# Kernel optimization log

Hardware: AMD Instinct MI355X
Metric: run time of the kernel (lower is better)

## Reference

```python
import jax, jax.numpy as jnp
import numpy as np

B, T = 8, 4096
EMBED_DIM = 128
ENGRAM_EMBED_DIM = 64
VOCAB_SIZES = [4096, 4096]
MAX_NGRAM = 3
NUM_HEADS = 2
N_STREAMS = 4
KERNEL = 4
TOTAL_NGRAMS = len(VOCAB_SIZES) * NUM_HEADS          # 4
INPUT_DIM = TOTAL_NGRAMS * ENGRAM_EMBED_DIM          # 256
TOTAL_SLOTS = sum(VOCAB_SIZES) * NUM_HEADS           # 16384


def setup_inputs() -> dict:
    key = jax.random.key(0)
    ks = jax.random.split(key, 10)
    x = jax.random.normal(ks[0], (B, T, N_STREAMS, EMBED_DIM), dtype=jnp.float32)
    input_ids = jax.random.randint(ks[1], (B, T), 0, 50257, dtype=jnp.int32)
    multipliers = jax.random.randint(ks[2], (MAX_NGRAM - 1, NUM_HEADS, MAX_NGRAM), 1, 10000, dtype=jnp.int32)
    embedding = jax.random.normal(ks[3], (TOTAL_SLOTS, ENGRAM_EMBED_DIM), dtype=jnp.float32) * 0.02
    val_W = jax.random.normal(ks[4], (EMBED_DIM, INPUT_DIM), dtype=jnp.float32) * 0.05
    val_b = jnp.zeros((EMBED_DIM,), jnp.float32)
    key_W = jax.random.normal(ks[5], (N_STREAMS, EMBED_DIM, INPUT_DIM), dtype=jnp.float32) * 0.05
    key_b = jnp.zeros((N_STREAMS, EMBED_DIM), jnp.float32)
    normq_w = jnp.ones((N_STREAMS, EMBED_DIM), jnp.float32)
    normk_w = jnp.ones((N_STREAMS, EMBED_DIM), jnp.float32)
    conv_w = jax.random.normal(ks[6], (N_STREAMS * EMBED_DIM, 1, KERNEL), dtype=jnp.float32) * 0.1
    convnorm_w = jnp.ones((N_STREAMS, EMBED_DIM), jnp.float32)
    return {"x": x, "input_ids": input_ids, "multipliers": multipliers,
            "embedding": embedding, "val_W": val_W, "val_b": val_b,
            "key_W": key_W, "key_b": key_b, "normq_w": normq_w,
            "normk_w": normk_w, "conv_w": conv_w, "convnorm_w": convnorm_w}


def rmsnorm(v, w):
    # torch nn.RMSNorm default eps = finfo(dtype).eps
    eps = jnp.finfo(v.dtype).eps
    return v * jax.lax.rsqrt(jnp.mean(v * v, axis=-1, keepdims=True) + eps) * w


def hash_ids_fn(input_ids, multipliers):
    padded = jnp.pad(input_ids, ((0, 0), (MAX_NGRAM - 1, 0)))            # [B, T+2]
    windows = jnp.stack([padded[:, i:i + T] for i in range(MAX_NGRAM)], axis=-1)  # [B,T,3]
    hashes = []
    for n_idx in range(MAX_NGRAM - 1):
        ngram_len = n_idx + 2
        grams = windows[:, :, MAX_NGRAM - ngram_len:]                    # [B,T,L]
        mults = multipliers[n_idx, :, :ngram_len]                        # [H,L]
        mixed = grams[:, :, None, :] * mults[None, None, :, :]           # [B,T,H,L]
        h = mixed[..., 0]
        for k in range(1, ngram_len):
            h = jnp.bitwise_xor(h, mixed[..., k])
        hashes.append(h % VOCAB_SIZES[n_idx])                            # [B,T,H]
    return jnp.concatenate(hashes, axis=2)                               # [B,T,4]


def engram_forward(x, input_ids, multipliers, embedding, val_W, val_b,
                   key_W, key_b, normq_w, normk_w, conv_w, convnorm_w):
    hids = hash_ids_fn(input_ids, multipliers)
    offsets = jnp.cumsum(jnp.array([0] + [v for v in VOCAB_SIZES for _ in range(NUM_HEADS)], jnp.int32))[:-1]
    ids = hids + offsets                                                 # [B,T,4]
    emb = embedding[ids].reshape(B, T, INPUT_DIM)                        # [B,T,256]
    v_base = emb @ val_W.T + val_b                                       # [B,T,128]
    k = rmsnorm(jnp.einsum('bte,gde->btgd', emb, key_W) + key_b, normk_w)  # [B,T,G,D]
    q = rmsnorm(x, normq_w)                                              # [B,T,G,D]
    score = jnp.sum(q * k, axis=-1, keepdims=True) / (EMBED_DIM ** 0.5)
    gates = jax.nn.sigmoid(score)                                        # [B,T,G,1]
    v_gated = v_base[:, :, None, :] * gates                              # [B,T,G,D]
    # ShortConv: per-chunk RMSNorm -> causal depthwise conv -> SiLU
    xn = rmsnorm(v_gated, convnorm_w).reshape(B, T, N_STREAMS * EMBED_DIM)
    x_bct = jnp.transpose(xn, (0, 2, 1))                                 # [B,C,T]
    x_bct = jnp.pad(x_bct, ((0, 0), (0, 0), (KERNEL - 1, 0)))            # causal left pad
    y_bct = jax.lax.conv_general_dilated(
        x_bct, conv_w, window_strides=(1,), padding='VALID',
        dimension_numbers=('NCH', 'OIH', 'NCH'),
        feature_group_count=N_STREAMS * EMBED_DIM)                       # [B,C,T]
    y = jax.nn.silu(y_bct)
    y = jnp.transpose(y, (0, 2, 1)).reshape(B, T, N_STREAMS, EMBED_DIM)
    return v_gated + y


def reference(x, input_ids, multipliers, embedding, val_W, val_b,
              key_W, key_b, normq_w, normk_w, conv_w, convnorm_w):
    return engram_forward(x, input_ids, multipliers, embedding, val_W, val_b,
                          key_W, key_b, normq_w, normk_w, conv_w, convnorm_w)
```

## Files before the change

kernel.cpp:

```cpp
#include <hip/hip_runtime.h>
#include <math.h>

#define EPS 1.1920928955078125e-07f

typedef __attribute__((ext_vector_type(8)))  short short8;
typedef __attribute__((ext_vector_type(4)))  short short4v;
typedef __attribute__((ext_vector_type(16))) float floatx16;

__device__ __forceinline__ float4 ld4(const float* __restrict__ p) { return *(const float4* __restrict__)p; }
__device__ __forceinline__ void   st4(float* __restrict__ p, float4 v) { *(float4* __restrict__)p = v; }

__device__ __forceinline__ unsigned short f2bf(float f) {
    union { float f; unsigned u; } v; v.f = f;
    unsigned r = v.u + 0x7fffu + ((v.u >> 16) & 1u);
    return (unsigned short)(r >> 16);
}

__global__ __launch_bounds__(256) void build_wb(const float* __restrict__ val_W,
                                                const float* __restrict__ key_W,
                                                unsigned short* __restrict__ WbF)
{
    int idx  = blockIdx.x * 256 + threadIdx.x;
    int lane = idx & 63;
    int ks   = (idx >> 6) & 15;
    int nt   = idx >> 10;
    int n = (nt << 5) + (lane & 31);
    int k = (ks << 4) + ((lane >> 5) << 3);
    const float* src = (n < 512) ? key_W + (size_t)n * 256 + k
                                 : val_W + (size_t)(n - 512) * 256 + k;
    float4 v0 = ld4(src), v1 = ld4(src + 4);
    unsigned short o[8] = { f2bf(v0.x), f2bf(v0.y), f2bf(v0.z), f2bf(v0.w),
                            f2bf(v1.x), f2bf(v1.y), f2bf(v1.z), f2bf(v1.w) };
    unsigned short* dst = WbF + (size_t)idx * 8;
    *(short4v*)dst       = *(short4v*)&o[0];
    *(short4v*)(dst + 4) = *(short4v*)&o[4];
}

__global__ __launch_bounds__(256) void build_ebf(const float* __restrict__ emb,
                                                 unsigned short* __restrict__ ebf)
{
    int idx = blockIdx.x * 256 + threadIdx.x;
    const float* src = emb + ((size_t)idx << 3);
    float4 v0 = ld4(src), v1 = ld4(src + 4);
    unsigned short o[8] = { f2bf(v0.x), f2bf(v0.y), f2bf(v0.z), f2bf(v0.w),
                            f2bf(v1.x), f2bf(v1.y), f2bf(v1.z), f2bf(v1.w) };
    unsigned short* dst = ebf + ((size_t)idx << 3);
    *(short4v*)dst       = *(short4v*)&o[0];
    *(short4v*)(dst + 4) = *(short4v*)&o[4];
}

__global__ __launch_bounds__(256, 4) void engram_gemm(
    const float* __restrict__ x,
    const int*   __restrict__ input_ids,
    const int*   __restrict__ mult,
    const unsigned short* __restrict__ ebf,
    const float* __restrict__ val_b,
    const float* __restrict__ key_b,
    const float* __restrict__ normq_w,
    const float* __restrict__ normk_w,
    const unsigned short* __restrict__ WbF,
    float* __restrict__ v_base,
    float* __restrict__ Gbuf,
    float* __restrict__ S2buf)
{
    __shared__ int   sids[32][4];
    __shared__ short AD[32 * 260];

    const int tid  = threadIdx.x;
    const int tok0 = blockIdx.x << 5;

    if (tid < 32) {
        int token = tok0 + tid;
        int b = token >> 12, t = token & 4095;
        const int* row = input_ids + (b << 12);
        unsigned g2 = (unsigned)row[t];
        unsigned g1 = (t >= 1) ? (unsigned)row[t - 1] : 0u;
        unsigned g0 = (t >= 2) ? (unsigned)row[t - 2] : 0u;
        sids[tid][0] = (int)(((g1 * (unsigned)mult[0]) ^ (g2 * (unsigned)mult[1])) & 4095u);
        sids[tid][1] = (int)((((g1 * (unsigned)mult[3]) ^ (g2 * (unsigned)mult[4])) & 4095u) + 4096u);
        sids[tid][2] = (int)((((g0 * (unsigned)mult[6]) ^ (g1 * (unsigned)mult[7]) ^ (g2 * (unsigned)mult[8])) & 4095u) + 8192u);
        sids[tid][3] = (int)((((g0 * (unsigned)mult[9]) ^ (g1 * (unsigned)mult[10]) ^ (g2 * (unsigned)mult[11])) & 4095u) + 12288u);
    }
    __syncthreads();

    #pragma unroll
    for (int it = 0; it < 4; ++it) {
        int f = (it << 8) + tid;
        int token = f >> 5, ch = f & 31;
        const unsigned short* src = ebf + ((size_t)sids[token][ch >> 3] << 6) + ((ch & 7) << 3);
        short4v lo = *(const short4v*)src;
        short4v hi = *(const short4v*)(src + 4);
        short* dst = AD + token * 260 + (ch << 3);
        *(short4v*)dst       = lo;
        *(short4v*)(dst + 4) = hi;
    }
    __syncthreads();

    const int lane = tid & 63;
    const int wv   = tid >> 6;
    const int half = lane >> 5;
    const int mrow = lane & 31;

    const short*  Ap = AD + mrow * 260 + (half << 3);
    const float4* Bf = (const float4*)WbF + lane;

    floatx16 acc[5];
    #pragma unroll
    for (int j = 0; j < 5; ++j)
        #pragma unroll
        for (int r = 0; r < 16; ++r) acc[j][r] = 0.f;

    #pragma unroll 2
    for (int ks = 0; ks < 16; ++ks) {
        short4v al = *(const short4v*)(Ap + (ks << 4));
        short4v ah = *(const short4v*)(Ap + (ks << 4) + 4);
        short8 a = { al[0], al[1], al[2], al[3], ah[0], ah[1], ah[2], ah[3] };
        #pragma unroll
        for (int j = 0; j < 5; ++j) {
            union { float4 f; short8 s; } ub;
            ub.f = Bf[(size_t)((((wv + (j << 2)) << 4) + ks) << 6)];
            acc[j] = __builtin_amdgcn_mfma_f32_32x32x16_bf16(a, ub.s, acc[j], 0, 0, 0);
        }
    }

    const int ty = tid >> 4, tx = tid & 15;
    const int tx8 = tx << 3;
    float* D = (float*)AD;
    const int colw = (wv << 5) + mrow;
    const int rb   = half << 2;

    #pragma unroll
    for (int c = 0; c < 5; ++c) {
        float4 xa0, xb0, xa1, xb1;
        if (c < 4) {
            const float* xp0 = x + ((((size_t)(tok0 + (ty << 1))     << 2) + c) << 7) + tx8;
            const float* xp1 = x + ((((size_t)(tok0 + (ty << 1) + 1) << 2) + c) << 7) + tx8;
            xa0 = ld4(xp0); xb0 = ld4(xp0 + 4);
            xa1 = ld4(xp1); xb1 = ld4(xp1 + 4);
        }
        __syncthreads();
        #pragma unroll
        for (int r = 0; r < 16; ++r) {
            int row = (r & 3) + ((r >> 2) << 3) + rb;
            D[row * 130 + colw] = acc[c][r];
        }
        __syncthreads();

        if (c < 4) {
            const int s = c;
            const float* kbp = key_b   + (s << 7) + tx8;
            const float* nqp = normq_w + (s << 7) + tx8;
            const float* nkp = normk_w + (s << 7) + tx8;
            float4 kba = ld4(kbp), kbb = ld4(kbp + 4);
            float4 nqa = ld4(nqp), nqb = ld4(nqp + 4);
            float4 nka = ld4(nkp), nkb = ld4(nkp + 4);
            float kb[8] = {kba.x, kba.y, kba.z, kba.w, kbb.x, kbb.y, kbb.z, kbb.w};
            float nq[8] = {nqa.x, nqa.y, nqa.z, nqa.w, nqb.x, nqb.y, nqb.z, nqb.w};
            float nk[8] = {nka.x, nka.y, nka.z, nka.w, nkb.x, nkb.y, nkb.z, nkb.w};
            #pragma unroll
            for (int j = 0; j < 2; ++j) {
                int t_loc = (ty << 1) + j;
                int token = tok0 + t_loc;
                const float* dp = D + t_loc * 130 + tx8;
                float kr[8]; float ks2 = 0.f;
                #pragma unroll
                for (int m = 0; m < 8; ++m) { kr[m] = dp[m] + kb[m]; ks2 += kr[m] * kr[m]; }
                float xv[8];
                if (j == 0) { xv[0]=xa0.x; xv[1]=xa0.y; xv[2]=xa0.z; xv[3]=xa0.w;
                              xv[4]=xb0.x; xv[5]=xb0.y; xv[6]=xb0.z; xv[7]=xb0.w; }
                else        { xv[0]=xa1.x; xv[1]=xa1.y; xv[2]=xa1.z; xv[3]=xa1.w;
                              xv[4]=xb1.x; xv[5]=xb1.y; xv[6]=xb1.z; xv[7]=xb1.w; }
                float xs2 = 0.f, dt = 0.f;
                #pragma unroll
                for (int m = 0; m < 8; ++m) { xs2 += xv[m] * xv[m]; dt += xv[m] * nq[m] * kr[m] * nk[m]; }
                #pragma unroll
                for (int off = 1; off < 16; off <<= 1) {
                    ks2 += __shfl_xor(ks2, off);
                    xs2 += __shfl_xor(xs2, off);
                    dt  += __shfl_xor(dt,  off);
                }
                float sc = dt * rsqrtf(xs2 * (1.f / 128.f) + EPS)
                              * rsqrtf(ks2 * (1.f / 128.f) + EPS) * 0.08838834764831845f;
                float gate = 1.f / (1.f + __expf(-sc));
                if (tx == 0) Gbuf[(token << 2) + s] = gate;
            }
        } else {
            const float* vbp = val_b + tx8;
            float4 vba = ld4(vbp), vbb = ld4(vbp + 4);
            float vb[8] = {vba.x, vba.y, vba.z, vba.w, vbb.x, vbb.y, vbb.z, vbb.w};
            #pragma unroll
            for (int j = 0; j < 2; ++j) {
                int t_loc = (ty << 1) + j;
                int token = tok0 + t_loc;
                const float* dp = D + t_loc * 130 + tx8;
                float v[8]; float s2 = 0.f;
                #pragma unroll
                for (int m = 0; m < 8; ++m) { v[m] = dp[m] + vb[m]; s2 += v[m] * v[m]; }
                #pragma unroll
                for (int off = 1; off < 16; off <<= 1) s2 += __shfl_xor(s2, off);
                float* vp = v_base + ((size_t)token << 7) + tx8;
                st4(vp,     make_float4(v[0], v[1], v[2], v[3]));
                st4(vp + 4, make_float4(v[4], v[5], v[6], v[7]));
                if (tx == 0) S2buf[token] = s2;
            }
        }
    }
}

__global__ __launch_bounds__(256) void engram_out(
    const float* __restrict__ v_base,
    const float* __restrict__ Gbuf,
    const float* __restrict__ S2buf,
    const float* __restrict__ conv_w,
    const float* __restrict__ convnorm_w,
    float* __restrict__ out)
{
    int idx   = blockIdx.x * 256 + threadIdx.x;
    int d4    = idx & 31;
    int token = idx >> 5;
    int t     = token & 4095;

    float vw[4][4];
    float fwin[4][4];
    float gcur[4];
    #pragma unroll
    for (int k = 0; k < 4; ++k) {
        int tt = t + k - 3;
        if (tt >= 0) {
            int tok2 = token + k - 3;
            float4 v = ld4(v_base + ((size_t)tok2 << 7) + (d4 << 2));
            vw[k][0] = v.x; vw[k][1] = v.y; vw[k][2] = v.z; vw[k][3] = v.w;
            float s2n = S2buf[tok2] * (1.f / 128.f);
            #pragma unroll
            for (int s = 0; s < 4; ++s) {
                float g = Gbuf[(tok2 << 2) + s];
                fwin[k][s] = g * rsqrtf(g * g * s2n + EPS);
                if (k == 3) gcur[s] = g;
            }
        } else {
            #pragma unroll
            for (int i = 0; i < 4; ++i) vw[k][i] = 0.f;
            #pragma unroll
            for (int s = 0; s < 4; ++s) fwin[k][s] = 0.f;
        }
    }

    #pragma unroll
    for (int s = 0; s < 4; ++s) {
        float4 cwv = ld4(convnorm_w + (s << 7) + (d4 << 2));
        float cw[4] = {cwv.x, cwv.y, cwv.z, cwv.w};
        float o[4];
        #pragma unroll
        for (int i = 0; i < 4; ++i) {
            const float* wp = conv_w + (size_t)(((s << 7) + (d4 << 2) + i) << 2);
            float4 w = ld4(wp);
            float a = w.x * vw[0][i] * fwin[0][s]
                    + w.y * vw[1][i] * fwin[1][s]
                    + w.z * vw[2][i] * fwin[2][s]
                    + w.w * vw[3][i] * fwin[3][s];
            float y = a * cw[i];
            o[i] = vw[3][i] * gcur[s] + y / (1.f + __expf(-y));
        }
        st4(out + ((size_t)((token << 2) + s) << 7) + (d4 << 2),
            make_float4(o[0], o[1], o[2], o[3]));
    }
}

extern "C" void kernel_launch(void* const* d_in, const int* in_sizes, int n_in,
                              void* d_out, int out_size, void* d_ws, size_t ws_size,
                              hipStream_t stream)
{
    const float* x          = (const float*)d_in[0];
    const int*   input_ids  = (const int*)d_in[1];
    const int*   mult       = (const int*)d_in[2];
    const float* embedding  = (const float*)d_in[3];
    const float* val_W      = (const float*)d_in[4];
    const float* val_b      = (const float*)d_in[5];
    const float* key_W      = (const float*)d_in[6];
    const float* key_b      = (const float*)d_in[7];
    const float* normq_w    = (const float*)d_in[8];
    const float* normk_w    = (const float*)d_in[9];
    const float* conv_w     = (const float*)d_in[10];
    const float* convnorm_w = (const float*)d_in[11];
    float* out = (float*)d_out;

    char* ws = (char*)d_ws;
    unsigned short* WbF = (unsigned short*)ws;
    unsigned short* ebf = (unsigned short*)(ws + 327680);
    float* v_base = (float*)(ws + 327680 + 2097152);
    float* Gbuf   = (float*)(ws + 327680 + 2097152 + 16777216);
    float* S2buf  = (float*)(ws + 327680 + 2097152 + 16777216 + 524288);

    build_wb<<<80, 256, 0, stream>>>(val_W, key_W, WbF);
    build_ebf<<<512, 256, 0, stream>>>(embedding, ebf);
    engram_gemm<<<1024, 256, 0, stream>>>(x, input_ids, mult, ebf, val_b, key_b,
                                          normq_w, normk_w, WbF, v_base, Gbuf, S2buf);
    engram_out<<<4096, 256, 0, stream>>>(v_base, Gbuf, S2buf, conv_w, convnorm_w, out);
}
```

Before: 185.9 us.

## Split GEMM by output tiles across blocks, merge pack kernels, reuse conv window

Merges the two bf16 pack kernels into one launch. Splits engram_gemm's five N-tiles across three block groups (two key tiles, two key tiles, one value tile), which triples the grid and lowers per-thread accumulator registers so the launch bound can rise to 6 blocks. Each block now repeats the embedding gather and A-tile staging, adding redundant gather traffic. engram_out gives each thread 4 consecutive tokens and 2 streams, so the 7-token window of v_base, S2 and gate loads is shared across outputs instead of reloaded per token.

```diff
diff --git a/kernel.cpp b/kernel.cpp
--- a/kernel.cpp
+++ b/kernel.cpp
@@ -16,40 +16,41 @@
     return (unsigned short)(r >> 16);
 }
 
-__global__ __launch_bounds__(256) void build_wb(const float* __restrict__ val_W,
-                                                const float* __restrict__ key_W,
-                                                unsigned short* __restrict__ WbF)
+__global__ __launch_bounds__(256) void build_pack(const float* __restrict__ val_W,
+                                                  const float* __restrict__ key_W,
+                                                  const float* __restrict__ emb,
+                                                  unsigned short* __restrict__ WbF,
+                                                  unsigned short* __restrict__ ebf)
 {
-    int idx  = blockIdx.x * 256 + threadIdx.x;
-    int lane = idx & 63;
-    int ks   = (idx >> 6) & 15;
-    int nt   = idx >> 10;
-    int n = (nt << 5) + (lane & 31);
-    int k = (ks << 4) + ((lane >> 5) << 3);
-    const float* src = (n < 512) ? key_W + (size_t)n * 256 + k
-                                 : val_W + (size_t)(n - 512) * 256 + k;
-    float4 v0 = ld4(src), v1 = ld4(src + 4);
-    unsigned short o[8] = { f2bf(v0.x), f2bf(v0.y), f2bf(v0.z), f2bf(v0.w),
-                            f2bf(v1.x), f2bf(v1.y), f2bf(v1.z), f2bf(v1.w) };
-    unsigned short* dst = WbF + (size_t)idx * 8;
-    *(short4v*)dst       = *(short4v*)&o[0];
-    *(short4v*)(dst + 4) = *(short4v*)&o[4];
-}
-
-__global__ __launch_bounds__(256) void build_ebf(const float* __restrict__ emb,
-                                                 unsigned short* __restrict__ ebf)
-{
-    int idx = blockIdx.x * 256 + threadIdx.x;
-    const float* src = emb + ((size_t)idx << 3);
-    float4 v0 = ld4(src), v1 = ld4(src + 4);
-    unsigned short o[8] = { f2bf(v0.x), f2bf(v0.y), f2bf(v0.z), f2bf(v0.w),
-                            f2bf(v1.x), f2bf(v1.y), f2bf(v1.z), f2bf(v1.w) };
-    unsigned short* dst = ebf + ((size_t)idx << 3);
-    *(short4v*)dst       = *(short4v*)&o[0];
-    *(short4v*)(dst + 4) = *(short4v*)&o[4];
-}
-
-__global__ __launch_bounds__(256, 4) void engram_gemm(
+    int bid = blockIdx.x;
+    if (bid < 80) {
+        int idx  = bid * 256 + threadIdx.x;
+        int lane = idx & 63;
+        int ks   = (idx >> 6) & 15;
+        int nt   = idx >> 10;
+        int n = (nt << 5) + (lane & 31);
+        int k = (ks << 4) + ((lane >> 5) << 3);
+        const float* src = (n < 512) ? key_W + (size_t)n * 256 + k
+                                     : val_W + (size_t)(n - 512) * 256 + k;
+        float4 v0 = ld4(src), v1 = ld4(src + 4);
+        unsigned short o[8] = { f2bf(v0.x), f2bf(v0.y), f2bf(v0.z), f2bf(v0.w),
+                                f2bf(v1.x), f2bf(v1.y), f2bf(v1.z), f2bf(v1.w) };
+        unsigned short* dst = WbF + (size_t)idx * 8;
+        *(short4v*)dst       = *(short4v*)&o[0];
+        *(short4v*)(dst + 4) = *(short4v*)&o[4];
+    } else {
+        int idx = (bid - 80) * 256 + threadIdx.x;
+        const float* src = emb + ((size_t)idx << 3);
+        float4 v0 = ld4(src), v1 = ld4(src + 4);
+        unsigned short o[8] = { f2bf(v0.x), f2bf(v0.y), f2bf(v0.z), f2bf(v0.w),
+                                f2bf(v1.x), f2bf(v1.y), f2bf(v1.z), f2bf(v1.w) };
+        unsigned short* dst = ebf + ((size_t)idx << 3);
+        *(short4v*)dst       = *(short4v*)&o[0];
+        *(short4v*)(dst + 4) = *(short4v*)&o[4];
+    }
+}
+
+__global__ __launch_bounds__(256, 6) void engram_gemm(
     const float* __restrict__ x,
     const int*   __restrict__ input_ids,
     const int*   __restrict__ mult,
@@ -67,7 +68,8 @@
     __shared__ short AD[32 * 260];
 
     const int tid  = threadIdx.x;
-    const int tok0 = blockIdx.x << 5;
+    const int part = blockIdx.x >> 10;
+    const int tok0 = (blockIdx.x & 1023) << 5;
 
     if (tid < 32) {
         int token = tok0 + tid;
@@ -104,50 +106,47 @@
     const short*  Ap = AD + mrow * 260 + (half << 3);
     const float4* Bf = (const float4*)WbF + lane;
 
-    floatx16 acc[5];
-    #pragma unroll
-    for (int j = 0; j < 5; ++j)
-        #pragma unroll
-        for (int r = 0; r < 16; ++r) acc[j][r] = 0.f;
-
-    #pragma unroll 2
-    for (int ks = 0; ks < 16; ++ks) {
-        short4v al = *(const short4v*)(Ap + (ks << 4));
-        short4v ah = *(const short4v*)(Ap + (ks << 4) + 4);
-        short8 a = { al[0], al[1], al[2], al[3], ah[0], ah[1], ah[2], ah[3] };
-        #pragma unroll
-        for (int j = 0; j < 5; ++j) {
-            union { float4 f; short8 s; } ub;
-            ub.f = Bf[(size_t)((((wv + (j << 2)) << 4) + ks) << 6)];
-            acc[j] = __builtin_amdgcn_mfma_f32_32x32x16_bf16(a, ub.s, acc[j], 0, 0, 0);
-        }
-    }
-
     const int ty = tid >> 4, tx = tid & 15;
     const int tx8 = tx << 3;
     float* D = (float*)AD;
     const int colw = (wv << 5) + mrow;
     const int rb   = half << 2;
 
-    #pragma unroll
-    for (int c = 0; c < 5; ++c) {
-        float4 xa0, xb0, xa1, xb1;
-        if (c < 4) {
-            const float* xp0 = x + ((((size_t)(tok0 + (ty << 1))     << 2) + c) << 7) + tx8;
-            const float* xp1 = x + ((((size_t)(tok0 + (ty << 1) + 1) << 2) + c) << 7) + tx8;
-            xa0 = ld4(xp0); xb0 = ld4(xp0 + 4);
-            xa1 = ld4(xp1); xb1 = ld4(xp1 + 4);
-        }
-        __syncthreads();
-        #pragma unroll
-        for (int r = 0; r < 16; ++r) {
-            int row = (r & 3) + ((r >> 2) << 3) + rb;
-            D[row * 130 + colw] = acc[c][r];
-        }
-        __syncthreads();
-
-        if (c < 4) {
-            const int s = c;
+    if (part < 2) {
+        const int c0 = part << 1;
+        floatx16 acc[2];
+        #pragma unroll
+        for (int r = 0; r < 16; ++r) { acc[0][r] = 0.f; acc[1][r] = 0.f; }
+
+        #pragma unroll 2
+        for (int ks = 0; ks < 16; ++ks) {
+            short4v al = *(const short4v*)(Ap + (ks << 4));
+            short4v ah = *(const short4v*)(Ap + (ks << 4) + 4);
+            short8 a = { al[0], al[1], al[2], al[3], ah[0], ah[1], ah[2], ah[3] };
+            #pragma unroll
+            for (int j = 0; j < 2; ++j) {
+                int nt = ((c0 + j) << 2) + wv;
+                union { float4 f; short8 s; } ub;
+                ub.f = Bf[(size_t)(((nt << 4) + ks) << 6)];
+                acc[j] = __builtin_amdgcn_mfma_f32_32x32x16_bf16(a, ub.s, acc[j], 0, 0, 0);
+            }
+        }
+
+        #pragma unroll
+        for (int j = 0; j < 2; ++j) {
+            const int s = c0 + j;
+            const float* xp0 = x + ((((size_t)(tok0 + (ty << 1))     << 2) + s) << 7) + tx8;
+            const float* xp1 = x + ((((size_t)(tok0 + (ty << 1) + 1) << 2) + s) << 7) + tx8;
+            float4 xa0 = ld4(xp0), xb0 = ld4(xp0 + 4);
+            float4 xa1 = ld4(xp1), xb1 = ld4(xp1 + 4);
+            __syncthreads();
+            #pragma unroll
+            for (int r = 0; r < 16; ++r) {
+                int row = (r & 3) + ((r >> 2) << 3) + rb;
+                D[row * 130 + colw] = acc[j][r];
+            }
+            __syncthreads();
+
             const float* kbp = key_b   + (s << 7) + tx8;
             const float* nqp = normq_w + (s << 7) + tx8;
             const float* nkp = normk_w + (s << 7) + tx8;
@@ -158,18 +157,18 @@
             float nq[8] = {nqa.x, nqa.y, nqa.z, nqa.w, nqb.x, nqb.y, nqb.z, nqb.w};
             float nk[8] = {nka.x, nka.y, nka.z, nka.w, nkb.x, nkb.y, nkb.z, nkb.w};
             #pragma unroll
-            for (int j = 0; j < 2; ++j) {
-                int t_loc = (ty << 1) + j;
+            for (int jj = 0; jj < 2; ++jj) {
+                int t_loc = (ty << 1) + jj;
                 int token = tok0 + t_loc;
                 const float* dp = D + t_loc * 130 + tx8;
                 float kr[8]; float ks2 = 0.f;
                 #pragma unroll
                 for (int m = 0; m < 8; ++m) { kr[m] = dp[m] + kb[m]; ks2 += kr[m] * kr[m]; }
                 float xv[8];
-                if (j == 0) { xv[0]=xa0.x; xv[1]=xa0.y; xv[2]=xa0.z; xv[3]=xa0.w;
-                              xv[4]=xb0.x; xv[5]=xb0.y; xv[6]=xb0.z; xv[7]=xb0.w; }
-                else        { xv[0]=xa1.x; xv[1]=xa1.y; xv[2]=xa1.z; xv[3]=xa1.w;
-                              xv[4]=xb1.x; xv[5]=xb1.y; xv[6]=xb1.z; xv[7]=xb1.w; }
+                if (jj == 0) { xv[0]=xa0.x; xv[1]=xa0.y; xv[2]=xa0.z; xv[3]=xa0.w;
+                               xv[4]=xb0.x; xv[5]=xb0.y; xv[6]=xb0.z; xv[7]=xb0.w; }
+                else         { xv[0]=xa1.x; xv[1]=xa1.y; xv[2]=xa1.z; xv[3]=xa1.w;
+                               xv[4]=xb1.x; xv[5]=xb1.y; xv[6]=xb1.z; xv[7]=xb1.w; }
                 float xs2 = 0.f, dt = 0.f;
                 #pragma unroll
                 for (int m = 0; m < 8; ++m) { xs2 += xv[m] * xv[m]; dt += xv[m] * nq[m] * kr[m] * nk[m]; }
@@ -184,30 +183,51 @@
                 float gate = 1.f / (1.f + __expf(-sc));
                 if (tx == 0) Gbuf[(token << 2) + s] = gate;
             }
-        } else {
-            const float* vbp = val_b + tx8;
-            float4 vba = ld4(vbp), vbb = ld4(vbp + 4);
-            float vb[8] = {vba.x, vba.y, vba.z, vba.w, vbb.x, vbb.y, vbb.z, vbb.w};
-            #pragma unroll
-            for (int j = 0; j < 2; ++j) {
-                int t_loc = (ty << 1) + j;
-                int token = tok0 + t_loc;
-                const float* dp = D + t_loc * 130 + tx8;
-                float v[8]; float s2 = 0.f;
-                #pragma unroll
-                for (int m = 0; m < 8; ++m) { v[m] = dp[m] + vb[m]; s2 += v[m] * v[m]; }
-                #pragma unroll
-                for (int off = 1; off < 16; off <<= 1) s2 += __shfl_xor(s2, off);
-                float* vp = v_base + ((size_t)token << 7) + tx8;
-                st4(vp,     make_float4(v[0], v[1], v[2], v[3]));
-                st4(vp + 4, make_float4(v[4], v[5], v[6], v[7]));
-                if (tx == 0) S2buf[token] = s2;
-            }
-        }
-    }
-}
-
-__global__ __launch_bounds__(256) void engram_out(
+        }
+    } else {
+        floatx16 acc;
+        #pragma unroll
+        for (int r = 0; r < 16; ++r) acc[r] = 0.f;
+        #pragma unroll 4
+        for (int ks = 0; ks < 16; ++ks) {
+            short4v al = *(const short4v*)(Ap + (ks << 4));
+            short4v ah = *(const short4v*)(Ap + (ks << 4) + 4);
+            short8 a = { al[0], al[1], al[2], al[3], ah[0], ah[1], ah[2], ah[3] };
+            int nt = 16 + wv;
+            union { float4 f; short8 s; } ub;
+            ub.f = Bf[(size_t)(((nt << 4) + ks) << 6)];
+            acc = __builtin_amdgcn_mfma_f32_32x32x16_bf16(a, ub.s, acc, 0, 0, 0);
+        }
+        __syncthreads();
+        #pragma unroll
+        for (int r = 0; r < 16; ++r) {
+            int row = (r & 3) + ((r >> 2) << 3) + rb;
+            D[row * 130 + colw] = acc[r];
+        }
+        __syncthreads();
+
+        const float* vbp = val_b + tx8;
+        float4 vba = ld4(vbp), vbb = ld4(vbp + 4);
+        float vb[8] = {vba.x, vba.y, vba.z, vba.w, vbb.x, vbb.y, vbb.z, vbb.w};
+        #pragma unroll
+        for (int jj = 0; jj < 2; ++jj) {
+            int t_loc = (ty << 1) + jj;
+            int token = tok0 + t_loc;
+            const float* dp = D + t_loc * 130 + tx8;
+            float v[8]; float s2 = 0.f;
+            #pragma unroll
+            for (int m = 0; m < 8; ++m) { v[m] = dp[m] + vb[m]; s2 += v[m] * v[m]; }
+            #pragma unroll
+            for (int off = 1; off < 16; off <<= 1) s2 += __shfl_xor(s2, off);
+            float* vp = v_base + ((size_t)token << 7) + tx8;
+            st4(vp,     make_float4(v[0], v[1], v[2], v[3]));
+            st4(vp + 4, make_float4(v[4], v[5], v[6], v[7]));
+            if (tx == 0) S2buf[token] = s2;
+        }
+    }
+}
+
+__global__ __launch_bounds__(256, 4) void engram_out(
     const float* __restrict__ v_base,
     const float* __restrict__ Gbuf,
     const float* __restrict__ S2buf,
@@ -215,54 +235,66 @@
     const float* __restrict__ convnorm_w,
     float* __restrict__ out)
 {
-    int idx   = blockIdx.x * 256 + threadIdx.x;
-    int d4    = idx & 31;
-    int token = idx >> 5;
-    int t     = token & 4095;
-
-    float vw[4][4];
-    float fwin[4][4];
-    float gcur[4];
+    int idx  = blockIdx.x * 256 + threadIdx.x;
+    int d4   = idx & 31;
+    int sp   = (idx >> 5) & 1;
+    int grp  = idx >> 6;
+    int tg0  = grp << 2;
+    int tsq0 = tg0 & 4095;
+    int s0   = sp << 1;
+
+    float v[7][4];
+    float fw[7][2];
+    float gq[4][2];
     #pragma unroll
-    for (int k = 0; k < 4; ++k) {
-        int tt = t + k - 3;
-        if (tt >= 0) {
-            int tok2 = token + k - 3;
-            float4 v = ld4(v_base + ((size_t)tok2 << 7) + (d4 << 2));
-            vw[k][0] = v.x; vw[k][1] = v.y; vw[k][2] = v.z; vw[k][3] = v.w;
-            float s2n = S2buf[tok2] * (1.f / 128.f);
-            #pragma unroll
-            for (int s = 0; s < 4; ++s) {
-                float g = Gbuf[(tok2 << 2) + s];
-                fwin[k][s] = g * rsqrtf(g * g * s2n + EPS);
-                if (k == 3) gcur[s] = g;
+    for (int j = 0; j < 7; ++j) {
+        if (tsq0 + j >= 3) {
+            int glob = tg0 - 3 + j;
+            float4 vv = ld4(v_base + ((size_t)glob << 7) + (d4 << 2));
+            v[j][0] = vv.x; v[j][1] = vv.y; v[j][2] = vv.z; v[j][3] = vv.w;
+            float s2n = S2buf[glob] * (1.f / 128.f);
+            #pragma unroll
+            for (int q = 0; q < 2; ++q) {
+                float g = Gbuf[(glob << 2) + s0 + q];
+                fw[j][q] = g * rsqrtf(g * g * s2n + EPS);
+                if (j >= 3) gq[j - 3][q] = g;
             }
         } else {
             #pragma unroll
-            for (int i = 0; i < 4; ++i) vw[k][i] = 0.f;
-            #pragma unroll
-            for (int s = 0; s < 4; ++s) fwin[k][s] = 0.f;
-        }
-    }
-
+            for (int i = 0; i < 4; ++i) v[j][i] = 0.f;
+            fw[j][0] = 0.f; fw[j][1] = 0.f;
+        }
+    }
+
+    float4 w[2][4];
+    float  cw[2][4];
     #pragma unroll
-    for (int s = 0; s < 4; ++s) {
-        float4 cwv = ld4(convnorm_w + (s << 7) + (d4 << 2));
-        float cw[4] = {cwv.x, cwv.y, cwv.z, cwv.w};
-        float o[4];
-        #pragma unroll
-        for (int i = 0; i < 4; ++i) {
-            const float* wp = conv_w + (size_t)(((s << 7) + (d4 << 2) + i) << 2);
-            float4 w = ld4(wp);
-            float a = w.x * vw[0][i] * fwin[0][s]
-                    + w.y * vw[1][i] * fwin[1][s]
-                    + w.z * vw[2][i] * fwin[2][s]
-                    + w.w * vw[3][i] * fwin[3][s];
-            float y = a * cw[i];
-            o[i] = vw[3][i] * gcur[s] + y / (1.f + __expf(-y));
-        }
-        st4(out + ((size_t)((token << 2) + s) << 7) + (d4 << 2),
-            make_float4(o[0], o[1], o[2], o[3]));
+    for (int q = 0; q < 2; ++q) {
+        float4 c = ld4(convnorm_w + ((s0 + q) << 7) + (d4 << 2));
+        cw[q][0] = c.x; cw[q][1] = c.y; cw[q][2] = c.z; cw[q][3] = c.w;
+        #pragma unroll
+        for (int i = 0; i < 4; ++i)
+            w[q][i] = ld4(conv_w + (size_t)(((((s0 + q) << 7) + (d4 << 2) + i)) << 2));
+    }
+
+    #pragma unroll
+    for (int t = 0; t < 4; ++t) {
+        int glob = tg0 + t;
+        #pragma unroll
+        for (int q = 0; q < 2; ++q) {
+            float o[4];
+            #pragma unroll
+            for (int i = 0; i < 4; ++i) {
+                float a = w[q][i].x * v[t][i]     * fw[t][q]
+                        + w[q][i].y * v[t + 1][i] * fw[t + 1][q]
+                        + w[q][i].z * v[t + 2][i] * fw[t + 2][q]
+                        + w[q][i].w * v[t + 3][i] * fw[t + 3][q];
+                float y = a * cw[q][i];
+                o[i] = v[t + 3][i] * gq[t][q] + y / (1.f + __expf(-y));
+            }
+            st4(out + ((size_t)((glob << 2) + s0 + q) << 7) + (d4 << 2),
+                make_float4(o[0], o[1], o[2], o[3]));
+        }
     }
 }
 
@@ -291,9 +323,8 @@
     float* Gbuf   = (float*)(ws + 327680 + 2097152 + 16777216);
     float* S2buf  = (float*)(ws + 327680 + 2097152 + 16777216 + 524288);
 
-    build_wb<<<80, 256, 0, stream>>>(val_W, key_W, WbF);
-    build_ebf<<<512, 256, 0, stream>>>(embedding, ebf);
-    engram_gemm<<<1024, 256, 0, stream>>>(x, input_ids, mult, ebf, val_b, key_b,
+    build_pack<<<592, 256, 0, stream>>>(val_W, key_W, embedding, WbF, ebf);
+    engram_gemm<<<3072, 256, 0, stream>>>(x, input_ids, mult, ebf, val_b, key_b,
                                           normq_w, normk_w, WbF, v_base, Gbuf, S2buf);
-    engram_out<<<4096, 256, 0, stream>>>(v_base, Gbuf, S2buf, conv_w, convnorm_w, out);
-}
+    engram_out<<<2048, 256, 0, stream>>>(v_base, Gbuf, S2buf, conv_w, convnorm_w, out);
+}
```

Measured after the change: 172.3 us. -7.3%, faster.
